# Performance work log

Hardware: AMD Instinct MI355X
Metric: run time of the kernel (lower is better)

## Reference

```python
import jax, jax.numpy as jnp
import numpy as np

N_NODES = 50000
N_EDGES = 800000
IN_DIM = 128
HID = 32
HEADS = 4
OUT_DIM = 64
NEG_SLOPE = 0.2  # DGL GATConv default


def setup_inputs() -> dict:
    key = jax.random.key(0)
    ks = jax.random.split(key, 20)

    def glorot(k, shape):
        fan = shape[0] + shape[-1]
        return (jax.random.normal(k, shape, jnp.float32) * np.sqrt(2.0 / fan)).astype(jnp.float32)

    inp = {
        "h": jax.random.normal(ks[0], (N_NODES, IN_DIM), jnp.float32),
        "src": jax.random.randint(ks[1], (N_EDGES,), 0, N_NODES, jnp.int32),
        "dst": jax.random.randint(ks[2], (N_EDGES,), 0, N_NODES, jnp.int32),
        # layer 0: in_dim -> hidden, HEADS heads, relu
        "W1": glorot(ks[3], (IN_DIM, HEADS * HID)),
        "al1": glorot(ks[4], (HEADS, HID)),
        "ar1": glorot(ks[5], (HEADS, HID)),
        "b1": jnp.zeros((HEADS * HID,), jnp.float32),
        # layer 1 (hidden): hidden*heads -> hidden, HEADS heads, relu
        "W2": glorot(ks[6], (HEADS * HID, HEADS * HID)),
        "al2": glorot(ks[7], (HEADS, HID)),
        "ar2": glorot(ks[8], (HEADS, HID)),
        "b2": jnp.zeros((HEADS * HID,), jnp.float32),
        # layer 2 (output): hidden*heads -> out_dim, 1 head, no activation
        "W3": glorot(ks[9], (HEADS * HID, OUT_DIM)),
        "al3": glorot(ks[10], (1, OUT_DIM)),
        "ar3": glorot(ks[11], (1, OUT_DIM)),
        "b3": jnp.zeros((OUT_DIM,), jnp.float32),
    }
    return inp


def gat_conv(h, src, dst, W, attn_l, attn_r, bias, heads, out_dim, use_relu):
    n = h.shape[0]
    feat = (h @ W).reshape(n, heads, out_dim)              # [N,H,D]
    el = jnp.sum(feat * attn_l[None], axis=-1)             # [N,H]
    er = jnp.sum(feat * attn_r[None], axis=-1)             # [N,H]
    e = jax.nn.leaky_relu(el[src] + er[dst], NEG_SLOPE)    # [E,H] per-edge logits
    # segment softmax over incoming edges of each dst node
    emax = jax.ops.segment_max(e, dst, num_segments=n)     # [N,H] (-inf for isolated nodes, never gathered)
    ee = jnp.exp(e - emax[dst])                            # [E,H]
    denom = jax.ops.segment_sum(ee, dst, num_segments=n)   # [N,H]
    alpha = ee / denom[dst]                                # [E,H]
    msg = feat[src] * alpha[:, :, None]                    # [E,H,D] gather + weight
    out = jax.ops.segment_sum(msg, dst, num_segments=n)    # [N,H,D] scatter-add
    out = out + bias.reshape(1, heads, out_dim)
    if use_relu:
        out = jax.nn.relu(out)
    return out.reshape(n, heads * out_dim)


def reference(h, src, dst, W1, al1, ar1, b1, W2, al2, ar2, b2, W3, al3, ar3, b3):
    # dropout is identity in eval mode
    h1 = gat_conv(h, src, dst, W1, al1, ar1, b1, HEADS, HID, True)
    h2 = gat_conv(h1, src, dst, W2, al2, ar2, b2, HEADS, HID, True)
    h3 = gat_conv(h2, src, dst, W3, al3, ar3, b3, 1, OUT_DIM, False)
    return h3
```

## Files before the change

kernel.cpp:

```cpp
#include <hip/hip_runtime.h>
#include <hip/hip_fp16.h>

#define NNODES 50000
#define NEDGES 800000
#define HISTB 256

__device__ __forceinline__ float leaky(float x) { return x >= 0.f ? x : 0.2f * x; }

typedef _Float16 f16x8 __attribute__((ext_vector_type(8)));
typedef float f32x4 __attribute__((ext_vector_type(4)));

struct __align__(8)  half4v { __half2 h0, h1; };
struct __align__(16) half8v { __half2 h0, h1, h2, h3; };

__global__ __launch_bounds__(256) void wtrans_k(const float* __restrict__ W1,
                                                const float* __restrict__ W2,
                                                const float* __restrict__ W3,
                                                __half* __restrict__ Wt) {
    int i = blockIdx.x * 256 + threadIdx.x;
    if (i < 16384) {
        int k = i >> 7, c = i & 127;
        Wt[c * 128 + k] = __float2half_rn(W1[i]);
    } else if (i < 32768) {
        int e = i - 16384, k = e >> 7, c = e & 127;
        Wt[16384 + c * 128 + k] = __float2half_rn(W2[e]);
    } else if (i < 40960) {
        int e = i - 32768, k = e >> 6, c = e & 63;
        Wt[32768 + c * 128 + k] = __float2half_rn(W3[e]);
    }
}

template<int F, int H, bool FP16IN, bool DO_HIST>
__global__ __launch_bounds__(256) void gemm_mfma_k(const void* __restrict__ Xv,
                                                   const __half* __restrict__ Wt,
                                                   const float* __restrict__ al,
                                                   const float* __restrict__ ar,
                                                   __half* __restrict__ Yh,
                                                   float* __restrict__ el,
                                                   float* __restrict__ er, int n,
                                                   int nGemm,
                                                   const int* __restrict__ dst,
                                                   int* __restrict__ cnt,
                                                   int* __restrict__ rank) {
    constexpr int K = 128;
    constexpr int NT = F / 16;
    constexpr int LDC = F + 8;

    if (DO_HIST && blockIdx.x >= nGemm) {
        int b = blockIdx.x - nGemm;
        for (int e = b * 256 + threadIdx.x; e < NEDGES; e += HISTB * 256)
            rank[e] = atomicAdd(&cnt[dst[e]], 1);
        return;
    }

    __shared__ __align__(16) __half Cs[64 * LDC];

    const int tid = threadIdx.x;
    const int wv = tid >> 6, lane = tid & 63;
    const int cl = lane & 15, kg = lane >> 4;
    const int r0 = blockIdx.x * 64;
    const int rowA = r0 + 16 * wv + cl;
    const int rA = rowA < n ? rowA : n - 1;

    f32x4 acc[NT];
    #pragma unroll
    for (int t = 0; t < NT; t++) acc[t] = (f32x4){0.f, 0.f, 0.f, 0.f};

    #pragma unroll
    for (int ks = 0; ks < K / 32; ks++) {
        f16x8 a;
        if constexpr (FP16IN) {
            a = *(const f16x8*)((const __half*)Xv + (size_t)rA * K + ks * 32 + kg * 8);
        } else {
            const float* Xp = (const float*)Xv + (size_t)rA * K + ks * 32 + kg * 8;
            float4 x0 = *(const float4*)Xp;
            float4 x1 = *(const float4*)(Xp + 4);
            a[0] = (_Float16)x0.x; a[1] = (_Float16)x0.y;
            a[2] = (_Float16)x0.z; a[3] = (_Float16)x0.w;
            a[4] = (_Float16)x1.x; a[5] = (_Float16)x1.y;
            a[6] = (_Float16)x1.z; a[7] = (_Float16)x1.w;
        }
        #pragma unroll
        for (int t = 0; t < NT; t++) {
            f16x8 b = *(const f16x8*)(Wt + (size_t)(16 * t + cl) * K + ks * 32 + kg * 8);
            acc[t] = __builtin_amdgcn_mfma_f32_16x16x32_f16(a, b, acc[t], 0, 0, 0);
        }
    }

    #pragma unroll
    for (int t = 0; t < NT; t++)
        #pragma unroll
        for (int j = 0; j < 4; j++)
            Cs[(16 * wv + 4 * kg + j) * LDC + 16 * t + cl] = __float2half_rn(acc[t][j]);
    __syncthreads();
    {
        constexpr int SEGS = F / 8;
        constexpr int RPS = 256 / SEGS;
        #pragma unroll
        for (int s = 0; s < 64 / RPS; s++) {
            int idx = s * 256 + tid;
            int row = idx / SEGS, seg = idx % SEGS;
            int grow = r0 + row;
            if (grow < n)
                *(half8v*)&Yh[(size_t)grow * F + seg * 8] =
                    *(const half8v*)&Cs[row * LDC + seg * 8];
        }
    }

    float alv[NT], arv[NT];
    #pragma unroll
    for (int t = 0; t < NT; t++) { alv[t] = al[16 * t + cl]; arv[t] = ar[16 * t + cl]; }

    if (H == 1) {
        float pl[4], pr[4];
        #pragma unroll
        for (int j = 0; j < 4; j++) {
            pl[j] = 0.f; pr[j] = 0.f;
            #pragma unroll
            for (int t = 0; t < NT; t++) { pl[j] += acc[t][j] * alv[t]; pr[j] += acc[t][j] * arv[t]; }
        }
        #pragma unroll
        for (int off = 1; off < 16; off <<= 1)
            #pragma unroll
            for (int j = 0; j < 4; j++) { pl[j] += __shfl_xor(pl[j], off); pr[j] += __shfl_xor(pr[j], off); }
        if (cl == 0)
            #pragma unroll
            for (int j = 0; j < 4; j++) {
                int row = r0 + 16 * wv + 4 * kg + j;
                if (row < n) { el[row] = pl[j]; er[row] = pr[j]; }
            }
    } else {
        float pl[4][4], pr[4][4];
        #pragma unroll
        for (int hh = 0; hh < 4; hh++)
            #pragma unroll
            for (int j = 0; j < 4; j++) {
                pl[hh][j] = acc[2 * hh][j] * alv[2 * hh] + acc[2 * hh + 1][j] * alv[2 * hh + 1];
                pr[hh][j] = acc[2 * hh][j] * arv[2 * hh] + acc[2 * hh + 1][j] * arv[2 * hh + 1];
            }
        #pragma unroll
        for (int off = 1; off < 16; off <<= 1)
            #pragma unroll
            for (int hh = 0; hh < 4; hh++)
                #pragma unroll
                for (int j = 0; j < 4; j++) {
                    pl[hh][j] += __shfl_xor(pl[hh][j], off);
                    pr[hh][j] += __shfl_xor(pr[hh][j], off);
                }
        if (cl == 0)
            #pragma unroll
            for (int j = 0; j < 4; j++) {
                int row = r0 + 16 * wv + 4 * kg + j;
                if (row < n)
                    #pragma unroll
                    for (int hh = 0; hh < 4; hh++) {
                        el[row * 4 + hh] = pl[hh][j];
                        er[row * 4 + hh] = pr[hh][j];
                    }
            }
    }
}

__global__ void scan_blk_k(const int* __restrict__ cnt, int* __restrict__ offs,
                           int* __restrict__ bsum, int n) {
    __shared__ int sm[256];
    int tid = threadIdx.x;
    int i = blockIdx.x * 256 + tid;
    int v = (i < n) ? cnt[i] : 0;
    sm[tid] = v;
    __syncthreads();
    for (int off = 1; off < 256; off <<= 1) {
        int t = (tid >= off) ? sm[tid - off] : 0;
        __syncthreads();
        sm[tid] += t;
        __syncthreads();
    }
    if (i < n) offs[i] = sm[tid] - v;
    if (tid == 255) bsum[blockIdx.x] = sm[255];
}

__global__ void scan_addtop_k(int* __restrict__ offs, const int* __restrict__ bsum,
                              int n, int nb) {
    __shared__ int sm[256];
    int tid = threadIdx.x;
    int v = (tid < nb) ? bsum[tid] : 0;
    sm[tid] = v;
    __syncthreads();
    for (int off = 1; off < 256; off <<= 1) {
        int t = (tid >= off) ? sm[tid - off] : 0;
        __syncthreads();
        sm[tid] += t;
        __syncthreads();
    }
    int prefix = (blockIdx.x > 0) ? sm[blockIdx.x - 1] : 0;
    int i = blockIdx.x * 256 + tid;
    if (i < n) offs[i] += prefix;
    if (i == 0) offs[n] = NEDGES;
}

__global__ void scatter_k(const int* __restrict__ src, const int* __restrict__ dst,
                          const int* __restrict__ rank, const int* __restrict__ offs,
                          int* __restrict__ esrc) {
    int e = blockIdx.x * blockDim.x + threadIdx.x;
    if (e < NEDGES) esrc[offs[dst[e]] + rank[e]] = src[e];
}

__global__ __launch_bounds__(256) void node_agg4_k(const int* __restrict__ offs,
                                                   const int* __restrict__ esrc,
                                                   const float* __restrict__ el,
                                                   const float* __restrict__ er,
                                                   const __half* __restrict__ feat,
                                                   const float* __restrict__ bias,
                                                   __half* __restrict__ out) {
    const int lane = threadIdx.x & 63;
    const int gw0 = (blockIdx.x * 256 + threadIdx.x) >> 6;
    const int NW = (gridDim.x * 256) >> 6;

    const int h  = lane & 3;
    const int q  = lane >> 4;
    const int cl = lane & 15;
    const int hd = cl >> 2;

    float4 ba = *(const float4*)&bias[8 * cl];
    float4 bb = *(const float4*)&bias[8 * cl + 4];

    for (int wid = gw0; wid < NNODES; wid += NW) {
        int beg = offs[wid], end = offs[wid + 1];
        float erh = er[wid * 4 + h];

        float acc[8] = {0.f, 0.f, 0.f, 0.f, 0.f, 0.f, 0.f, 0.f};
        float dsum = 0.f;
        for (int base = beg; base < end; base += 16) {
            int rem = end - base;
            if (rem > 16) rem = 16;
            int sv = 0;
            if (lane < rem) sv = esrc[base + lane];
            int se = __shfl(sv, lane >> 2);
            float p = 0.f;
            if ((lane >> 2) < rem)
                p = __expf(leaky(el[se * 4 + h] + erh));
            dsum += p;
            #pragma unroll
            for (int e = 0; e < 16 && e < rem; e += 4) {
                int eidx = e + q;
                int s = __shfl(sv, eidx);
                float a = __shfl(p, eidx * 4 + hd);
                half8v hv = *(const half8v*)&feat[(size_t)s * 128 + 8 * cl];
                float2 f0 = __half22float2(hv.h0);
                float2 f1 = __half22float2(hv.h1);
                float2 f2 = __half22float2(hv.h2);
                float2 f3 = __half22float2(hv.h3);
                acc[0] += f0.x * a; acc[1] += f0.y * a;
                acc[2] += f1.x * a; acc[3] += f1.y * a;
                acc[4] += f2.x * a; acc[5] += f2.y * a;
                acc[6] += f3.x * a; acc[7] += f3.y * a;
            }
        }
        #pragma unroll
        for (int c = 0; c < 8; c++) {
            acc[c] += __shfl_xor(acc[c], 16);
            acc[c] += __shfl_xor(acc[c], 32);
        }
        #pragma unroll
        for (int off = 4; off < 64; off <<= 1) dsum += __shfl_xor(dsum, off);
        float dh = __shfl(dsum, hd);
        float inv = dh > 0.f ? 1.f / dh : 0.f;
        if (q == 0) {
            float v0 = fmaxf(acc[0] * inv + ba.x, 0.f), v1 = fmaxf(acc[1] * inv + ba.y, 0.f);
            float v2 = fmaxf(acc[2] * inv + ba.z, 0.f), v3 = fmaxf(acc[3] * inv + ba.w, 0.f);
            float v4 = fmaxf(acc[4] * inv + bb.x, 0.f), v5 = fmaxf(acc[5] * inv + bb.y, 0.f);
            float v6 = fmaxf(acc[6] * inv + bb.z, 0.f), v7 = fmaxf(acc[7] * inv + bb.w, 0.f);
            half8v hv;
            hv.h0 = __halves2half2(__float2half_rn(v0), __float2half_rn(v1));
            hv.h1 = __halves2half2(__float2half_rn(v2), __float2half_rn(v3));
            hv.h2 = __halves2half2(__float2half_rn(v4), __float2half_rn(v5));
            hv.h3 = __halves2half2(__float2half_rn(v6), __float2half_rn(v7));
            *(half8v*)&out[(size_t)wid * 128 + 8 * cl] = hv;
        }
    }
}

__global__ __launch_bounds__(256) void node_agg1_k(const int* __restrict__ offs,
                                                   const int* __restrict__ esrc,
                                                   const float* __restrict__ el,
                                                   const float* __restrict__ er,
                                                   const __half* __restrict__ feat,
                                                   const float* __restrict__ bias,
                                                   float* __restrict__ out) {
    const int lane = threadIdx.x & 63;
    const int gw0 = (blockIdx.x * 256 + threadIdx.x) >> 6;
    const int NW = (gridDim.x * 256) >> 6;

    const int q  = lane >> 4;
    const int cl = lane & 15;
    float4 b4 = *(const float4*)&bias[4 * cl];

    for (int wid = gw0; wid < NNODES; wid += NW) {
        int beg = offs[wid], end = offs[wid + 1];
        float erd = er[wid];

        float acc[4] = {0.f, 0.f, 0.f, 0.f};
        float dsum = 0.f;
        for (int base = beg; base < end; base += 64) {
            int rem = end - base;
            if (rem > 64) rem = 64;
            int sv = 0;
            float p = 0.f;
            if (lane < rem) {
                sv = esrc[base + lane];
                p = __expf(leaky(el[sv] + erd));
            }
            dsum += p;
            #pragma unroll 4
            for (int e = 0; e < rem; e += 4) {
                int eidx = e + q;
                int s = __shfl(sv, eidx);
                float a = __shfl(p, eidx);
                half4v hv = *(const half4v*)&feat[(size_t)s * 64 + 4 * cl];
                float2 f0 = __half22float2(hv.h0);
                float2 f1 = __half22float2(hv.h1);
                acc[0] += f0.x * a; acc[1] += f0.y * a;
                acc[2] += f1.x * a; acc[3] += f1.y * a;
            }
        }
        #pragma unroll
        for (int c = 0; c < 4; c++) {
            acc[c] += __shfl_xor(acc[c], 16);
            acc[c] += __shfl_xor(acc[c], 32);
        }
        #pragma unroll
        for (int off = 1; off < 64; off <<= 1) dsum += __shfl_xor(dsum, off);
        float inv = dsum > 0.f ? 1.f / dsum : 0.f;
        if (q == 0) {
            *(float4*)&out[(size_t)wid * 64 + 4 * cl] =
                make_float4(acc[0] * inv + b4.x, acc[1] * inv + b4.y,
                            acc[2] * inv + b4.z, acc[3] * inv + b4.w);
        }
    }
}

extern "C" void kernel_launch(void* const* d_in, const int* in_sizes, int n_in,
                              void* d_out, int out_size, void* d_ws, size_t ws_size,
                              hipStream_t stream) {
    const float* h   = (const float*)d_in[0];
    const int*   src = (const int*)d_in[1];
    const int*   dst = (const int*)d_in[2];
    const float* W1  = (const float*)d_in[3];
    const float* al1 = (const float*)d_in[4];
    const float* ar1 = (const float*)d_in[5];
    const float* b1  = (const float*)d_in[6];
    const float* W2  = (const float*)d_in[7];
    const float* al2 = (const float*)d_in[8];
    const float* ar2 = (const float*)d_in[9];
    const float* b2  = (const float*)d_in[10];
    const float* W3  = (const float*)d_in[11];
    const float* al3 = (const float*)d_in[12];
    const float* ar3 = (const float*)d_in[13];
    const float* b3  = (const float*)d_in[14];
    float* out = (float*)d_out;

    const int n = NNODES;
    __half* feat16 = (__half*)d_ws;
    __half* hbuf16 = feat16 + (size_t)n * 128;
    float*  el     = (float*)(hbuf16 + (size_t)n * 128);
    float*  er     = el + (size_t)n * 4;
    int*    cnt    = (int*)(er + (size_t)n * 4);
    int*    offs   = cnt + n;
    int*    esrc   = offs + (n + 1);
    int*    bsum   = esrc + NEDGES;
    int*    rank   = bsum + 256;
    __half* wt     = (__half*)(rank + NEDGES);
    __half* wt1 = wt, *wt2 = wt + 16384, *wt3 = wt + 32768;

    const int gemmBlocks = (n + 63) / 64;
    const int nBlk = (n + 255) / 256;
    const int eBlk = (NEDGES + 255) / 256;
    const int aggBlk = 2048;

    hipMemsetAsync(cnt, 0, (size_t)n * sizeof(int), stream);
    wtrans_k<<<160, 256, 0, stream>>>(W1, W2, W3, wt);

    gemm_mfma_k<128, 4, false, true><<<gemmBlocks + HISTB, 256, 0, stream>>>(
        h, wt1, al1, ar1, feat16, el, er, n, gemmBlocks, dst, cnt, rank);

    scan_blk_k<<<nBlk, 256, 0, stream>>>(cnt, offs, bsum, n);
    scan_addtop_k<<<nBlk, 256, 0, stream>>>(offs, bsum, n, nBlk);
    scatter_k<<<eBlk, 256, 0, stream>>>(src, dst, rank, offs, esrc);

    node_agg4_k<<<aggBlk, 256, 0, stream>>>(offs, esrc, el, er, feat16, b1, hbuf16);

    gemm_mfma_k<128, 4, true, false><<<gemmBlocks, 256, 0, stream>>>(
        hbuf16, wt2, al2, ar2, feat16, el, er, n, gemmBlocks, nullptr, nullptr, nullptr);
    node_agg4_k<<<aggBlk, 256, 0, stream>>>(offs, esrc, el, er, feat16, b2, hbuf16);

    gemm_mfma_k<64, 1, true, false><<<gemmBlocks, 256, 0, stream>>>(
        hbuf16, wt3, al3, ar3, feat16, el, er, n, gemmBlocks, nullptr, nullptr, nullptr);
    node_agg1_k<<<aggBlk, 256, 0, stream>>>(offs, esrc, el, er, feat16, b3, out);
}
```

Before: 217.2 us.

## Process two nodes per wavefront in aggregation and fuse count reset into init

The aggregation kernels now split each 64-lane wavefront into two 32-lane halves, each handling its own destination node, with the edge chunk halved and cross-lane reductions shortened. With about 16 incoming edges per node, this is meant to cut idle lanes and loop overhead per node. The separate memset of the degree counters is folded into the weight-transpose kernel, removing one launch. Half-wave processing adds divergence between the two halves when their nodes have different in-degrees.

Measured after the change: 218.6 us. No clear change (+0.7%).

```diff
diff --git a/kernel.cpp b/kernel.cpp
--- a/kernel.cpp
+++ b/kernel.cpp
@@ -13,11 +13,13 @@
 struct __align__(8)  half4v { __half2 h0, h1; };
 struct __align__(16) half8v { __half2 h0, h1, h2, h3; };
 
-__global__ __launch_bounds__(256) void wtrans_k(const float* __restrict__ W1,
-                                                const float* __restrict__ W2,
-                                                const float* __restrict__ W3,
-                                                __half* __restrict__ Wt) {
+__global__ __launch_bounds__(256) void init_k(const float* __restrict__ W1,
+                                              const float* __restrict__ W2,
+                                              const float* __restrict__ W3,
+                                              __half* __restrict__ Wt,
+                                              int* __restrict__ cnt) {
     int i = blockIdx.x * 256 + threadIdx.x;
+    if (i < NNODES) cnt[i] = 0;
     if (i < 16384) {
         int k = i >> 7, c = i & 127;
         Wt[c * 128 + k] = __float2half_rn(W1[i]);
@@ -95,9 +97,8 @@
     __syncthreads();
     {
         constexpr int SEGS = F / 8;
-        constexpr int RPS = 256 / SEGS;
-        #pragma unroll
-        for (int s = 0; s < 64 / RPS; s++) {
+        #pragma unroll
+        for (int s = 0; s < 64 * SEGS / 256; s++) {
             int idx = s * 256 + tid;
             int row = idx / SEGS, seg = idx % SEGS;
             int grow = r0 + row;
@@ -213,38 +214,45 @@
                                                    const float* __restrict__ bias,
                                                    __half* __restrict__ out) {
     const int lane = threadIdx.x & 63;
-    const int gw0 = (blockIdx.x * 256 + threadIdx.x) >> 6;
-    const int NW = (gridDim.x * 256) >> 6;
-
-    const int h  = lane & 3;
-    const int q  = lane >> 4;
-    const int cl = lane & 15;
+    const int half = lane >> 5;
+    const int hl = lane & 31;
+    const int hb = half * 32;
+    const int gp0 = (blockIdx.x * 256 + threadIdx.x) >> 6;
+    const int NP = (gridDim.x * 256) >> 6;
+
+    const int h  = hl & 3;
+    const int q  = hl >> 4;
+    const int cl = hl & 15;
     const int hd = cl >> 2;
 
     float4 ba = *(const float4*)&bias[8 * cl];
     float4 bb = *(const float4*)&bias[8 * cl + 4];
 
-    for (int wid = gw0; wid < NNODES; wid += NW) {
-        int beg = offs[wid], end = offs[wid + 1];
-        float erh = er[wid * 4 + h];
+    for (int pair = gp0; pair * 2 < NNODES; pair += NP) {
+        int wid = pair * 2 + half;
+        bool valid = wid < NNODES;
+        int beg = 0, end = 0;
+        float erh = 0.f;
+        if (valid) { beg = offs[wid]; end = offs[wid + 1]; erh = er[wid * 4 + h]; }
 
         float acc[8] = {0.f, 0.f, 0.f, 0.f, 0.f, 0.f, 0.f, 0.f};
         float dsum = 0.f;
-        for (int base = beg; base < end; base += 16) {
+        for (int base = beg; base < end; base += 8) {
             int rem = end - base;
-            if (rem > 16) rem = 16;
+            if (rem > 8) rem = 8;
             int sv = 0;
-            if (lane < rem) sv = esrc[base + lane];
-            int se = __shfl(sv, lane >> 2);
+            if (hl < rem) sv = esrc[base + hl];
+            int se = __shfl(sv, hb + (hl >> 2));
             float p = 0.f;
-            if ((lane >> 2) < rem)
+            if ((hl >> 2) < rem)
                 p = __expf(leaky(el[se * 4 + h] + erh));
             dsum += p;
             #pragma unroll
-            for (int e = 0; e < 16 && e < rem; e += 4) {
+            for (int e = 0; e < 8; e += 2) {
+                if (e >= rem) break;
                 int eidx = e + q;
-                int s = __shfl(sv, eidx);
-                float a = __shfl(p, eidx * 4 + hd);
+                int s = __shfl(sv, hb + eidx);
+                float a = __shfl(p, hb + eidx * 4 + hd);
                 half8v hv = *(const half8v*)&feat[(size_t)s * 128 + 8 * cl];
                 float2 f0 = __half22float2(hv.h0);
                 float2 f1 = __half22float2(hv.h1);
@@ -257,15 +265,13 @@
             }
         }
         #pragma unroll
-        for (int c = 0; c < 8; c++) {
-            acc[c] += __shfl_xor(acc[c], 16);
-            acc[c] += __shfl_xor(acc[c], 32);
-        }
-        #pragma unroll
-        for (int off = 4; off < 64; off <<= 1) dsum += __shfl_xor(dsum, off);
-        float dh = __shfl(dsum, hd);
+        for (int c = 0; c < 8; c++) acc[c] += __shfl_xor(acc[c], 16);
+        dsum += __shfl_xor(dsum, 4);
+        dsum += __shfl_xor(dsum, 8);
+        dsum += __shfl_xor(dsum, 16);
+        float dh = __shfl(dsum, hb + hd);
         float inv = dh > 0.f ? 1.f / dh : 0.f;
-        if (q == 0) {
+        if (q == 0 && valid) {
             float v0 = fmaxf(acc[0] * inv + ba.x, 0.f), v1 = fmaxf(acc[1] * inv + ba.y, 0.f);
             float v2 = fmaxf(acc[2] * inv + ba.z, 0.f), v3 = fmaxf(acc[3] * inv + ba.w, 0.f);
             float v4 = fmaxf(acc[4] * inv + bb.x, 0.f), v5 = fmaxf(acc[5] * inv + bb.y, 0.f);
@@ -288,34 +294,40 @@
                                                    const float* __restrict__ bias,
                                                    float* __restrict__ out) {
     const int lane = threadIdx.x & 63;
-    const int gw0 = (blockIdx.x * 256 + threadIdx.x) >> 6;
-    const int NW = (gridDim.x * 256) >> 6;
-
-    const int q  = lane >> 4;
-    const int cl = lane & 15;
+    const int half = lane >> 5;
+    const int hl = lane & 31;
+    const int hb = half * 32;
+    const int gp0 = (blockIdx.x * 256 + threadIdx.x) >> 6;
+    const int NP = (gridDim.x * 256) >> 6;
+
+    const int q  = hl >> 4;
+    const int cl = hl & 15;
     float4 b4 = *(const float4*)&bias[4 * cl];
 
-    for (int wid = gw0; wid < NNODES; wid += NW) {
-        int beg = offs[wid], end = offs[wid + 1];
-        float erd = er[wid];
+    for (int pair = gp0; pair * 2 < NNODES; pair += NP) {
+        int wid = pair * 2 + half;
+        bool valid = wid < NNODES;
+        int beg = 0, end = 0;
+        float erd = 0.f;
+        if (valid) { beg = offs[wid]; end = offs[wid + 1]; erd = er[wid]; }
 
         float acc[4] = {0.f, 0.f, 0.f, 0.f};
         float dsum = 0.f;
-        for (int base = beg; base < end; base += 64) {
+        for (int base = beg; base < end; base += 32) {
             int rem = end - base;
-            if (rem > 64) rem = 64;
+            if (rem > 32) rem = 32;
             int sv = 0;
             float p = 0.f;
-            if (lane < rem) {
-                sv = esrc[base + lane];
+            if (hl < rem) {
+                sv = esrc[base + hl];
                 p = __expf(leaky(el[sv] + erd));
             }
             dsum += p;
             #pragma unroll 4
-            for (int e = 0; e < rem; e += 4) {
+            for (int e = 0; e < rem; e += 2) {
                 int eidx = e + q;
-                int s = __shfl(sv, eidx);
-                float a = __shfl(p, eidx);
+                int s = __shfl(sv, hb + eidx);
+                float a = __shfl(p, hb + eidx);
                 half4v hv = *(const half4v*)&feat[(size_t)s * 64 + 4 * cl];
                 float2 f0 = __half22float2(hv.h0);
                 float2 f1 = __half22float2(hv.h1);
@@ -324,14 +336,11 @@
             }
         }
         #pragma unroll
-        for (int c = 0; c < 4; c++) {
-            acc[c] += __shfl_xor(acc[c], 16);
-            acc[c] += __shfl_xor(acc[c], 32);
-        }
-        #pragma unroll
-        for (int off = 1; off < 64; off <<= 1) dsum += __shfl_xor(dsum, off);
+        for (int c = 0; c < 4; c++) acc[c] += __shfl_xor(acc[c], 16);
+        #pragma unroll
+        for (int off = 1; off < 32; off <<= 1) dsum += __shfl_xor(dsum, off);
         float inv = dsum > 0.f ? 1.f / dsum : 0.f;
-        if (q == 0) {
+        if (q == 0 && valid) {
             *(float4*)&out[(size_t)wid * 64 + 4 * cl] =
                 make_float4(acc[0] * inv + b4.x, acc[1] * inv + b4.y,
                             acc[2] * inv + b4.z, acc[3] * inv + b4.w);
@@ -377,8 +386,7 @@
     const int eBlk = (NEDGES + 255) / 256;
     const int aggBlk = 2048;
 
-    hipMemsetAsync(cnt, 0, (size_t)n * sizeof(int), stream);
-    wtrans_k<<<160, 256, 0, stream>>>(W1, W2, W3, wt);
+    init_k<<<nBlk, 256, 0, stream>>>(W1, W2, W3, wt, cnt);
 
     gemm_mfma_k<128, 4, false, true><<<gemmBlocks + HISTB, 256, 0, stream>>>(
         h, wt1, al1, ar1, feat16, el, er, n, gemmBlocks, dst, cnt, rank);
```

## Split GEMM columns across waves and fold count reset into init kernel

Applied to the files above, without the earlier changes.

The MFMA GEMM gains a CSPLIT template parameter, so with CSPLIT=2 each block handles 32 rows and two waves share each 16-row strip, each computing half of the output columns (two of the four heads). This doubles the block count for the 128-wide layers and halves per-wave accumulator registers, aiming for better occupancy and load balance. The count-array memset is merged into the weight-transpose kernel, removing one launch. The cost is that the A tile is loaded twice per row strip.

After: 217.2 us (median of 2 runs). Within noise of the previous version (+0.0%).

```diff
diff --git a/kernel.cpp b/kernel.cpp
--- a/kernel.cpp
+++ b/kernel.cpp
@@ -13,11 +13,13 @@
 struct __align__(8)  half4v { __half2 h0, h1; };
 struct __align__(16) half8v { __half2 h0, h1, h2, h3; };
 
-__global__ __launch_bounds__(256) void wtrans_k(const float* __restrict__ W1,
-                                                const float* __restrict__ W2,
-                                                const float* __restrict__ W3,
-                                                __half* __restrict__ Wt) {
+__global__ __launch_bounds__(256) void init_k(const float* __restrict__ W1,
+                                              const float* __restrict__ W2,
+                                              const float* __restrict__ W3,
+                                              __half* __restrict__ Wt,
+                                              int* __restrict__ cnt) {
     int i = blockIdx.x * 256 + threadIdx.x;
+    if (i < NNODES) cnt[i] = 0;
     if (i < 16384) {
         int k = i >> 7, c = i & 127;
         Wt[c * 128 + k] = __float2half_rn(W1[i]);
@@ -30,7 +32,7 @@
     }
 }
 
-template<int F, int H, bool FP16IN, bool DO_HIST>
+template<int F, int H, bool FP16IN, bool DO_HIST, int CSPLIT>
 __global__ __launch_bounds__(256) void gemm_mfma_k(const void* __restrict__ Xv,
                                                    const __half* __restrict__ Wt,
                                                    const float* __restrict__ al,
@@ -43,7 +45,8 @@
                                                    int* __restrict__ cnt,
                                                    int* __restrict__ rank) {
     constexpr int K = 128;
-    constexpr int NT = F / 16;
+    constexpr int ROWS = 64 / CSPLIT;
+    constexpr int NTW = F / 16 / CSPLIT;
     constexpr int LDC = F + 8;
 
     if (DO_HIST && blockIdx.x >= nGemm) {
@@ -53,18 +56,20 @@
         return;
     }
 
-    __shared__ __align__(16) __half Cs[64 * LDC];
+    __shared__ __align__(16) __half Cs[ROWS * LDC];
 
     const int tid = threadIdx.x;
     const int wv = tid >> 6, lane = tid & 63;
+    const int rs = wv / CSPLIT;
+    const int ch = wv % CSPLIT;
     const int cl = lane & 15, kg = lane >> 4;
-    const int r0 = blockIdx.x * 64;
-    const int rowA = r0 + 16 * wv + cl;
+    const int r0 = blockIdx.x * ROWS;
+    const int rowA = r0 + 16 * rs + cl;
     const int rA = rowA < n ? rowA : n - 1;
 
-    f32x4 acc[NT];
+    f32x4 acc[NTW];
     #pragma unroll
-    for (int t = 0; t < NT; t++) acc[t] = (f32x4){0.f, 0.f, 0.f, 0.f};
+    for (int t = 0; t < NTW; t++) acc[t] = (f32x4){0.f, 0.f, 0.f, 0.f};
 
     #pragma unroll
     for (int ks = 0; ks < K / 32; ks++) {
@@ -81,23 +86,24 @@
             a[6] = (_Float16)x1.z; a[7] = (_Float16)x1.w;
         }
         #pragma unroll
-        for (int t = 0; t < NT; t++) {
-            f16x8 b = *(const f16x8*)(Wt + (size_t)(16 * t + cl) * K + ks * 32 + kg * 8);
+        for (int t = 0; t < NTW; t++) {
+            int tg = ch * NTW + t;
+            f16x8 b = *(const f16x8*)(Wt + (size_t)(16 * tg + cl) * K + ks * 32 + kg * 8);
             acc[t] = __builtin_amdgcn_mfma_f32_16x16x32_f16(a, b, acc[t], 0, 0, 0);
         }
     }
 
     #pragma unroll
-    for (int t = 0; t < NT; t++)
+    for (int t = 0; t < NTW; t++)
         #pragma unroll
         for (int j = 0; j < 4; j++)
-            Cs[(16 * wv + 4 * kg + j) * LDC + 16 * t + cl] = __float2half_rn(acc[t][j]);
+            Cs[(16 * rs + 4 * kg + j) * LDC + (ch * NTW + t) * 16 + cl] =
+                __float2half_rn(acc[t][j]);
     __syncthreads();
     {
         constexpr int SEGS = F / 8;
-        constexpr int RPS = 256 / SEGS;
-        #pragma unroll
-        for (int s = 0; s < 64 / RPS; s++) {
+        #pragma unroll
+        for (int s = 0; s < ROWS * SEGS / 256; s++) {
             int idx = s * 256 + tid;
             int row = idx / SEGS, seg = idx % SEGS;
             int grow = r0 + row;
@@ -107,9 +113,12 @@
         }
     }
 
-    float alv[NT], arv[NT];
+    float alv[NTW], arv[NTW];
     #pragma unroll
-    for (int t = 0; t < NT; t++) { alv[t] = al[16 * t + cl]; arv[t] = ar[16 * t + cl]; }
+    for (int t = 0; t < NTW; t++) {
+        alv[t] = al[(ch * NTW + t) * 16 + cl];
+        arv[t] = ar[(ch * NTW + t) * 16 + cl];
+    }
 
     if (H == 1) {
         float pl[4], pr[4];
@@ -117,7 +126,7 @@
         for (int j = 0; j < 4; j++) {
             pl[j] = 0.f; pr[j] = 0.f;
             #pragma unroll
-            for (int t = 0; t < NT; t++) { pl[j] += acc[t][j] * alv[t]; pr[j] += acc[t][j] * arv[t]; }
+            for (int t = 0; t < NTW; t++) { pl[j] += acc[t][j] * alv[t]; pr[j] += acc[t][j] * arv[t]; }
         }
         #pragma unroll
         for (int off = 1; off < 16; off <<= 1)
@@ -126,13 +135,14 @@
         if (cl == 0)
             #pragma unroll
             for (int j = 0; j < 4; j++) {
-                int row = r0 + 16 * wv + 4 * kg + j;
+                int row = r0 + 16 * rs + 4 * kg + j;
                 if (row < n) { el[row] = pl[j]; er[row] = pr[j]; }
             }
     } else {
-        float pl[4][4], pr[4][4];
-        #pragma unroll
-        for (int hh = 0; hh < 4; hh++)
+        constexpr int HPW = NTW / 2;
+        float pl[HPW][4], pr[HPW][4];
+        #pragma unroll
+        for (int hh = 0; hh < HPW; hh++)
             #pragma unroll
             for (int j = 0; j < 4; j++) {
                 pl[hh][j] = acc[2 * hh][j] * alv[2 * hh] + acc[2 * hh + 1][j] * alv[2 * hh + 1];
@@ -141,7 +151,7 @@
         #pragma unroll
         for (int off = 1; off < 16; off <<= 1)
             #pragma unroll
-            for (int hh = 0; hh < 4; hh++)
+            for (int hh = 0; hh < HPW; hh++)
                 #pragma unroll
                 for (int j = 0; j < 4; j++) {
                     pl[hh][j] += __shfl_xor(pl[hh][j], off);
@@ -150,12 +160,12 @@
         if (cl == 0)
             #pragma unroll
             for (int j = 0; j < 4; j++) {
-                int row = r0 + 16 * wv + 4 * kg + j;
+                int row = r0 + 16 * rs + 4 * kg + j;
                 if (row < n)
                     #pragma unroll
-                    for (int hh = 0; hh < 4; hh++) {
-                        el[row * 4 + hh] = pl[hh][j];
-                        er[row * 4 + hh] = pr[hh][j];
+                    for (int hh = 0; hh < HPW; hh++) {
+                        el[row * H + ch * HPW + hh] = pl[hh][j];
+                        er[row * H + ch * HPW + hh] = pr[hh][j];
                     }
             }
     }
@@ -372,16 +382,16 @@
     __half* wt     = (__half*)(rank + NEDGES);
     __half* wt1 = wt, *wt2 = wt + 16384, *wt3 = wt + 32768;
 
-    const int gemmBlocks = (n + 63) / 64;
+    const int gemm32 = (n + 31) / 32;
+    const int gemm64 = (n + 63) / 64;
     const int nBlk = (n + 255) / 256;
     const int eBlk = (NEDGES + 255) / 256;
     const int aggBlk = 2048;
 
-    hipMemsetAsync(cnt, 0, (size_t)n * sizeof(int), stream);
-    wtrans_k<<<160, 256, 0, stream>>>(W1, W2, W3, wt);
-
-    gemm_mfma_k<128, 4, false, true><<<gemmBlocks + HISTB, 256, 0, stream>>>(
-        h, wt1, al1, ar1, feat16, el, er, n, gemmBlocks, dst, cnt, rank);
+    init_k<<<nBlk, 256, 0, stream>>>(W1, W2, W3, wt, cnt);
+
+    gemm_mfma_k<128, 4, false, true, 2><<<gemm32 + HISTB, 256, 0, stream>>>(
+        h, wt1, al1, ar1, feat16, el, er, n, gemm32, dst, cnt, rank);
 
     scan_blk_k<<<nBlk, 256, 0, stream>>>(cnt, offs, bsum, n);
     scan_addtop_k<<<nBlk, 256, 0, stream>>>(offs, bsum, n, nBlk);
@@ -389,11 +399,11 @@
 
     node_agg4_k<<<aggBlk, 256, 0, stream>>>(offs, esrc, el, er, feat16, b1, hbuf16);
 
-    gemm_mfma_k<128, 4, true, false><<<gemmBlocks, 256, 0, stream>>>(
-        hbuf16, wt2, al2, ar2, feat16, el, er, n, gemmBlocks, nullptr, nullptr, nullptr);
+    gemm_mfma_k<128, 4, true, false, 2><<<gemm32, 256, 0, stream>>>(
+        hbuf16, wt2, al2, ar2, feat16, el, er, n, gemm32, nullptr, nullptr, nullptr);
     node_agg4_k<<<aggBlk, 256, 0, stream>>>(offs, esrc, el, er, feat16, b2, hbuf16);
 
-    gemm_mfma_k<64, 1, true, false><<<gemmBlocks, 256, 0, stream>>>(
-        hbuf16, wt3, al3, ar3, feat16, el, er, n, gemmBlocks, nullptr, nullptr, nullptr);
+    gemm_mfma_k<64, 1, true, false, 1><<<gemm64, 256, 0, stream>>>(
+        hbuf16, wt3, al3, ar3, feat16, el, er, n, gemm64, nullptr, nullptr, nullptr);
     node_agg1_k<<<aggBlk, 256, 0, stream>>>(offs, esrc, el, er, feat16, b3, out);
 }
```
